# Kernel optimization log

Measured on AMD Instinct MI355X. Metric: run time of the kernel, lower is better.

Reference implementation:

```python
import jax, jax.numpy as jnp
import numpy as np

M, N, L = 1024, 1024, 64  # spatial rows, spatial cols, spectral bands


def setup_inputs() -> dict:
    key = jax.random.key(0)
    k1, k2 = jax.random.split(key)
    x = jax.random.uniform(k1, (1, M, N, L), dtype=jnp.float32)   # spectral cube
    ca = jax.random.uniform(k2, (1, M, N, 1), dtype=jnp.float32)  # coded aperture
    return {"x": x, "ca": ca}


def reference(x, ca):
    """CASSI forward: y[m, n+l] += x[m, n, l] * ca[m, n].

    Faithful to forward_cassi's loop of L pad+add ops, but expressed as a
    single vectorized scatter-add along the dispersion diagonal.
    """
    _, m, n, l = x.shape
    y1 = (x * ca)[0]                                       # (M, N, L) coded cube
    # destination column for band l at column n is n + l
    idx = jnp.arange(n)[:, None] + jnp.arange(l)[None, :]  # (N, L)
    y2 = jnp.zeros((m, n + l - 1), dtype=x.dtype).at[:, idx].add(y1)
    return y2[None, :, :, None]                            # (1, M, N+L-1, 1)
```

## Files before the change

### kernel.cpp

```cpp
#include <hip/hip_runtime.h>


#define CASSI_M 1024
#define CASSI_N 1024
#define CASSI_L 64
#define CASSI_OUTW (CASSI_N + CASSI_L - 1)

constexpr int CN = 128;
constexpr int P = CASSI_L + 1;
constexpr int NCHUNK = CASSI_N / CN;
constexpr int OPT = 5;

__global__ __launch_bounds__(256) void cassi_gather_kernel(
    const float* __restrict__ x, const float* __restrict__ ca,
    float* __restrict__ out) {
    __shared__ float xs[CN * P];

    const int m = blockIdx.x;
    const int t = threadIdx.x;

    float acc[OPT];
#pragma unroll
    for (int j = 0; j < OPT; ++j) acc[j] = 0.0f;

    const float* __restrict__ xrow = x + (size_t)m * (CASSI_N * CASSI_L);
    const float* __restrict__ carow = ca + (size_t)m * CASSI_N;

    for (int c = 0; c < NCHUNK; ++c) {
        const int n0 = c * CN;

#pragma unroll
        for (int s = 0; s < (CN * CASSI_L) / (256 * 4); ++s) {
            const int f = (s * 256 + t) * 4;
            const int nrel = f >> 6;
            const int l = f & 63;
            const float4 v = *reinterpret_cast<const float4*>(xrow + n0 * CASSI_L + f);
            const float cav = carow[n0 + nrel];
            float* dst = &xs[nrel * P + l];
            dst[0] = v.x * cav;
            dst[1] = v.y * cav;
            dst[2] = v.z * cav;
            dst[3] = v.w * cav;
        }
        __syncthreads();

#pragma unroll
        for (int j = 0; j < OPT; ++j) {
            const int o = t + 256 * j;
            if (o < CASSI_OUTW) {
                int llo = o - (n0 + CN - 1); if (llo < 0) llo = 0;
                int lhi = o - n0;            if (lhi > 63) lhi = 63;
                if (llo == 0 && lhi == 63) {
                    const int b = o - n0;
                    float s0 = 0.0f, s1 = 0.0f;
#pragma unroll
                    for (int l = 0; l < 64; l += 2) {
                        s0 += xs[(b - l) * P + l];
                        s1 += xs[(b - l - 1) * P + l + 1];
                    }
                    acc[j] += s0 + s1;
                } else {
                    for (int l = llo; l <= lhi; ++l)
                        acc[j] += xs[(o - n0 - l) * P + l];
                }
            }
        }
        __syncthreads();
    }

    float* __restrict__ orow = out + (size_t)m * CASSI_OUTW;
#pragma unroll
    for (int j = 0; j < OPT; ++j) {
        const int o = t + 256 * j;
        if (o < CASSI_OUTW) orow[o] = acc[j];
    }
}

extern "C" void kernel_launch(void* const* d_in, const int* in_sizes, int n_in,
                              void* d_out, int out_size, void* d_ws, size_t ws_size,
                              hipStream_t stream) {
    const float* x  = (const float*)d_in[0];
    const float* ca = (const float*)d_in[1];
    float* out = (float*)d_out;
    (void)in_sizes; (void)n_in; (void)out_size; (void)d_ws; (void)ws_size;

    cassi_gather_kernel<<<CASSI_M, 256, 0, stream>>>(x, ca, out);
}
```

Baseline: 369.2 us.

## Register-prefetch next x chunk while computing current chunk diagonal sums

```diff
diff --git a/kernel.cpp b/kernel.cpp
--- a/kernel.cpp
+++ b/kernel.cpp
@@ -10,8 +10,9 @@
 constexpr int P = CASSI_L + 1;
 constexpr int NCHUNK = CASSI_N / CN;
 constexpr int OPT = 5;
+constexpr int SPC = (CN * CASSI_L) / (256 * 4);
 
-__global__ __launch_bounds__(256) void cassi_gather_kernel(
+__global__ __launch_bounds__(256) void cassi_pipe_kernel(
     const float* __restrict__ x, const float* __restrict__ ca,
     float* __restrict__ out) {
     __shared__ float xs[CN * P];
@@ -19,39 +20,60 @@
     const int m = blockIdx.x;
     const int t = threadIdx.x;
 
+    const float* __restrict__ xrow = x + (size_t)m * (CASSI_N * CASSI_L);
+    const float* __restrict__ carow = ca + (size_t)m * CASSI_N;
+
+    float4 vbuf[SPC];
+    float  cbuf[SPC];
+
+#pragma unroll
+    for (int s = 0; s < SPC; ++s) {
+        const int f = (s * 256 + t) * 4;
+        vbuf[s] = *reinterpret_cast<const float4*>(xrow + f);
+        cbuf[s] = carow[f >> 6];
+    }
+
     float acc[OPT];
 #pragma unroll
     for (int j = 0; j < OPT; ++j) acc[j] = 0.0f;
 
-    const float* __restrict__ xrow = x + (size_t)m * (CASSI_N * CASSI_L);
-    const float* __restrict__ carow = ca + (size_t)m * CASSI_N;
-
     for (int c = 0; c < NCHUNK; ++c) {
         const int n0 = c * CN;
 
+        __syncthreads();
 #pragma unroll
-        for (int s = 0; s < (CN * CASSI_L) / (256 * 4); ++s) {
+        for (int s = 0; s < SPC; ++s) {
             const int f = (s * 256 + t) * 4;
             const int nrel = f >> 6;
             const int l = f & 63;
-            const float4 v = *reinterpret_cast<const float4*>(xrow + n0 * CASSI_L + f);
-            const float cav = carow[n0 + nrel];
+            const float cv = cbuf[s];
             float* dst = &xs[nrel * P + l];
-            dst[0] = v.x * cav;
-            dst[1] = v.y * cav;
-            dst[2] = v.z * cav;
-            dst[3] = v.w * cav;
+            dst[0] = vbuf[s].x * cv;
+            dst[1] = vbuf[s].y * cv;
+            dst[2] = vbuf[s].z * cv;
+            dst[3] = vbuf[s].w * cv;
         }
         __syncthreads();
+
+        if (c + 1 < NCHUNK) {
+            const float* __restrict__ src = xrow + (size_t)(n0 + CN) * CASSI_L;
+            const float* __restrict__ csrc = carow + (n0 + CN);
+#pragma unroll
+            for (int s = 0; s < SPC; ++s) {
+                const int f = (s * 256 + t) * 4;
+                vbuf[s] = *reinterpret_cast<const float4*>(src + f);
+                cbuf[s] = csrc[f >> 6];
+            }
+        }
 
 #pragma unroll
         for (int j = 0; j < OPT; ++j) {
             const int o = t + 256 * j;
             if (o < CASSI_OUTW) {
-                int llo = o - (n0 + CN - 1); if (llo < 0) llo = 0;
-                int lhi = o - n0;            if (lhi > 63) lhi = 63;
+                const int b = o - n0;
+                int llo = b - (CN - 1); if (llo < 0) llo = 0;
+                int lhi = b;            if (lhi > 63) lhi = 63;
                 if (llo == 0 && lhi == 63) {
-                    const int b = o - n0;
                     float s0 = 0.0f, s1 = 0.0f;
 #pragma unroll
                     for (int l = 0; l < 64; l += 2) {
@@ -59,13 +81,14 @@
                         s1 += xs[(b - l - 1) * P + l + 1];
                     }
                     acc[j] += s0 + s1;
-                } else {
+                } else if (llo <= lhi) {
+                    float s = 0.0f;
                     for (int l = llo; l <= lhi; ++l)
-                        acc[j] += xs[(o - n0 - l) * P + l];
+                        s += xs[(b - l) * P + l];
+                    acc[j] += s;
                 }
             }
         }
-        __syncthreads();
     }
 
     float* __restrict__ orow = out + (size_t)m * CASSI_OUTW;
@@ -84,5 +107,5 @@
     float* out = (float*)d_out;
     (void)in_sizes; (void)n_in; (void)out_size; (void)d_ws; (void)ws_size;
 
-    cassi_gather_kernel<<<CASSI_M, 256, 0, stream>>>(x, ca, out);
+    cassi_pipe_kernel<<<CASSI_M, 256, 0, stream>>>(x, ca, out);
 }
```

Measured after the change: 370.8 us. Within noise of the previous version (+0.4%).
